# Kernel tuning notes

Hardware: AMD Instinct MI355X
Metric: run time of the kernel (lower is better)

Reference implementation:

```python
import jax, jax.numpy as jnp
import numpy as np

# Spec constants (from init_kwargs)
NUM_ANCHORS = 5
NUM_CLASSES = 80
FM_H = 19
FM_W = 19
MAX_OBJECT = 50
NOOBJECT_SCALE = 1.0
OBJECT_SCALE = 5.0
BACKGROUND_THRESHOLD = 0.6
COORD_SCALE = 1.0
CLASS_SCALE = 1.0


def _iou_cwh(a, b):
    """IoU for boxes in (cx, cy, w, h) format; broadcasts over leading dims.
    Matches bbox_iou(..., x1y1x2y2=False) in the torch repo (0 when no overlap)."""
    ax1, ax2 = a[..., 0] - a[..., 2] * 0.5, a[..., 0] + a[..., 2] * 0.5
    ay1, ay2 = a[..., 1] - a[..., 3] * 0.5, a[..., 1] + a[..., 3] * 0.5
    bx1, bx2 = b[..., 0] - b[..., 2] * 0.5, b[..., 0] + b[..., 2] * 0.5
    by1, by2 = b[..., 1] - b[..., 3] * 0.5, b[..., 1] + b[..., 3] * 0.5
    uw = jnp.maximum(ax2, bx2) - jnp.minimum(ax1, bx1)
    uh = jnp.maximum(ay2, by2) - jnp.minimum(ay1, by1)
    cw = a[..., 2] + b[..., 2] - uw
    ch = a[..., 3] + b[..., 3] - uh
    inter = jnp.where((cw > 0) & (ch > 0), cw * ch, 0.0)
    union = a[..., 2] * a[..., 3] + b[..., 2] * b[..., 3] - inter
    return inter / jnp.maximum(union, 1e-12)


def setup_inputs() -> dict:
    key = jax.random.key(0)
    k1, k2, k3, k4, k5 = jax.random.split(key, 5)
    B, A, C, H, W, T = 64, NUM_ANCHORS, NUM_CLASSES, FM_H, FM_W, MAX_OBJECT
    output = jax.random.normal(k1, (B, A * (5 + C), H, W), jnp.float32) * 0.5
    # targets: per object (class, cx, cy, w, h), normalized to [0,1]; list ends at first cx == 0
    cls_t = jax.random.randint(k2, (B, T), 0, C).astype(jnp.float32)
    xy = jax.random.uniform(k3, (B, T, 2), jnp.float32, minval=0.1, maxval=0.9)
    wh = jax.random.uniform(k4, (B, T, 2), jnp.float32, minval=0.05, maxval=0.4)
    nvalid = jax.random.randint(k5, (B,), 1, T + 1)
    valid = (jnp.arange(T)[None, :] < nvalid[:, None]).astype(jnp.float32)
    tgt = jnp.concatenate([cls_t[..., None], xy, wh], axis=-1) * valid[..., None]
    target = tgt.reshape(B, T * 5)
    anchors = jnp.array([[1.3221, 1.73145], [3.19275, 4.00944], [5.05587, 8.09892],
                         [9.47112, 4.84053], [11.2364, 10.0071]], jnp.float32)
    return {"output": output, "target": target, "anchors": anchors}


def reference(output, target, anchors):
    B = output.shape[0]
    A, C, H, W, T = NUM_ANCHORS, NUM_CLASSES, FM_H, FM_W, MAX_OBJECT
    out = output.reshape(B, A, 5 + C, H, W)
    x = jax.nn.sigmoid(out[:, :, 0])
    y = jax.nn.sigmoid(out[:, :, 1])
    w = out[:, :, 2]
    h = out[:, :, 3]
    conf = jax.nn.sigmoid(out[:, :, 4])
    cls_logits = jnp.transpose(out[:, :, 5:], (0, 1, 3, 4, 2))  # [B,A,H,W,C]

    # decoded predicted boxes in grid units (detached for target building, as in torch)
    px = x + jnp.arange(W, dtype=x.dtype)[None, None, None, :]
    py = y + jnp.arange(H, dtype=x.dtype)[None, None, :, None]
    pw = jnp.exp(w) * anchors[None, :, 0, None, None]
    ph = jnp.exp(h) * anchors[None, :, 1, None, None]
    pred = jax.lax.stop_gradient(jnp.stack([px, py, pw, ph], axis=-1))  # [B,A,H,W,4]

    tgt = target.reshape(B, T, 5)
    cls_t = tgt[..., 0]
    gx = tgt[..., 1] * W
    gy = tgt[..., 2] * H
    gw = tgt[..., 3] * W
    gh = tgt[..., 4] * H
    # break-at-first-zero semantics of the torch loop
    valid = jnp.cumprod((tgt[..., 1] != 0).astype(jnp.int32), axis=1).astype(bool)  # [B,T]

    gt_boxes = jnp.stack([gx, gy, gw, gh], axis=-1)  # [B,T,4]
    # all-pairs pred-vs-gt IoU (replaces per-object python loop)
    pred_flat = pred.reshape(B, A * H * W, 4)
    ious = _iou_cwh(pred_flat[:, :, None, :], gt_boxes[:, None, :, :])  # [B,N,T]
    best_iou = jnp.max(jnp.where(valid[:, None, :], ious, 0.0), axis=-1)  # [B,N]
    conf_mask = jnp.where(best_iou > BACKGROUND_THRESHOLD, 0.0, NOOBJECT_SCALE)
    conf_mask = conf_mask.reshape(B, A, H, W)

    # best anchor per gt: IoU of (w,h) boxes centered at origin
    aw = anchors[:, 0][None, None, :]
    ah = anchors[:, 1][None, None, :]
    inter_a = jnp.minimum(gw[..., None], aw) * jnp.minimum(gh[..., None], ah)
    union_a = gw[..., None] * gh[..., None] + aw * ah - inter_a
    best_n = jnp.argmax(inter_a / jnp.maximum(union_a, 1e-12), axis=-1)  # [B,T]

    gi = jnp.clip(gx.astype(jnp.int32), 0, W - 1)
    gj = jnp.clip(gy.astype(jnp.int32), 0, H - 1)
    bidx = jnp.arange(B)[:, None]
    pred_sel = pred[bidx, best_n, gj, gi]  # [B,T,4]
    iou_obj = _iou_cwh(gt_boxes, pred_sel)  # [B,T]

    N = B * A * H * W
    flat = ((bidx * A + best_n) * H + gj) * W + gi  # [B,T]
    flat = jnp.where(valid, flat, N).reshape(-1)  # invalid -> out of range, dropped

    def scat(vals):
        return jnp.zeros((N,), jnp.float32).at[flat].set(
            vals.reshape(-1), mode="drop").reshape(B, A, H, W)

    coord_mask = scat(jnp.ones_like(gx))
    cls_mask = coord_mask
    conf_mask = conf_mask.reshape(-1).at[flat].set(
        jnp.full((B * T,), OBJECT_SCALE, jnp.float32), mode="drop").reshape(B, A, H, W)
    tx = scat(gx - gi.astype(gx.dtype))
    ty = scat(gy - gj.astype(gy.dtype))
    tw = scat(jnp.log(jnp.maximum(gw, 1e-12) / anchors[best_n, 0]))
    th = scat(jnp.log(jnp.maximum(gh, 1e-12) / anchors[best_n, 1]))
    tconf = scat(iou_obj)
    tcls = scat(cls_t)

    # losses (sum reduction, matching MSELoss/CrossEntropyLoss(size_average=False))
    loss_x = COORD_SCALE * jnp.sum((coord_mask * (x - tx)) ** 2) / 2.0
    loss_y = COORD_SCALE * jnp.sum((coord_mask * (y - ty)) ** 2) / 2.0
    loss_w = COORD_SCALE * jnp.sum((coord_mask * (w - tw)) ** 2) / 2.0
    loss_h = COORD_SCALE * jnp.sum((coord_mask * (h - th)) ** 2) / 2.0
    sq = jnp.sqrt(conf_mask)
    loss_conf = jnp.sum((sq * (conf - tconf)) ** 2) / 2.0
    ce = -jnp.take_along_axis(jax.nn.log_softmax(cls_logits, axis=-1),
                              tcls.astype(jnp.int32)[..., None], axis=-1)[..., 0]
    loss_cls = CLASS_SCALE * jnp.sum(cls_mask * ce)
    return loss_x + loss_y + loss_w + loss_h + loss_conf + loss_cls
```

## Files before the change

### kernel.cpp

```cpp
#include <hip/hip_runtime.h>
#include <math.h>

#define NUM_ANCHORS 5
#define NUM_CLASSES 80
#define FM_H 19
#define FM_W 19
#define MAX_OBJECT 50
#define HW (FM_H * FM_W)
#define CELLS_PER_B (NUM_ANCHORS * HW)
#define CH (5 + NUM_CLASSES)
#define BLOCKS_PER_B ((CELLS_PER_B + 255) / 256)
#define NOOBJECT_SCALE 1.0f
#define OBJECT_SCALE 5.0f
#define BACKGROUND_THRESHOLD 0.6f

struct GTEntry {
    float gx, gy, gw, gh;
    float tx, ty, tw, th;
    int   acell;
    int   cls;
};

__device__ inline float frcp(float v) { return __builtin_amdgcn_rcpf(v); }
__device__ inline float fsigmoid(float v) { return frcp(1.0f + __expf(-v)); }

__device__ inline float iou_cwh(float ax, float ay, float aw, float ah,
                                float bx, float by, float bw, float bh) {
    float ax1 = ax - aw * 0.5f, ax2 = ax + aw * 0.5f;
    float ay1 = ay - ah * 0.5f, ay2 = ay + ah * 0.5f;
    float bx1 = bx - bw * 0.5f, bx2 = bx + bw * 0.5f;
    float by1 = by - bh * 0.5f, by2 = by + bh * 0.5f;
    float uw = fmaxf(ax2, bx2) - fminf(ax1, bx1);
    float uh = fmaxf(ay2, by2) - fminf(ay1, by1);
    float cw = aw + bw - uw;
    float chh = ah + bh - uh;
    float inter = (cw > 0.0f && chh > 0.0f) ? cw * chh : 0.0f;
    float uni = aw * ah + bw * bh - inter;
    return inter * frcp(fmaxf(uni, 1e-12f));
}

__global__ __launch_bounds__(256) void yolov2_main(
    const float* __restrict__ out,
    const float* __restrict__ target,
    const float* __restrict__ anchors,
    float* __restrict__ partial)
{
    const int b    = blockIdx.x / BLOCKS_PER_B;
    const int blk  = blockIdx.x % BLOCKS_PER_B;
    const int cell = blk * 256 + threadIdx.x;
    const int lane = threadIdx.x & 63;
    const int wid  = threadIdx.x >> 6;

    __shared__ float tg[MAX_OBJECT * 5];
    __shared__ float anc[NUM_ANCHORS * 2];
    __shared__ GTEntry g[MAX_OBJECT];
    __shared__ int   nv_sh;
    __shared__ int   n_obj;
    __shared__ int   entries[MAX_OBJECT];
    __shared__ float wsum[4];

    for (int i = threadIdx.x; i < MAX_OBJECT * 5; i += blockDim.x)
        tg[i] = target[b * MAX_OBJECT * 5 + i];
    if (threadIdx.x < NUM_ANCHORS * 2)
        anc[threadIdx.x] = anchors[threadIdx.x];
    if (threadIdx.x == 0) n_obj = 0;
    __syncthreads();

    if (threadIdx.x < 64) {
        unsigned long long m =
            __ballot(threadIdx.x < MAX_OBJECT && tg[threadIdx.x * 5 + 1] != 0.0f);
        if (threadIdx.x == 0) nv_sh = __popcll(m);
    }

    if (threadIdx.x < MAX_OBJECT) {
        const int t = threadIdx.x;
        float cls = tg[t * 5 + 0];
        float gx = tg[t * 5 + 1] * (float)FM_W;
        float gy = tg[t * 5 + 2] * (float)FM_H;
        float gw = tg[t * 5 + 3] * (float)FM_W;
        float gh = tg[t * 5 + 4] * (float)FM_H;
        int bn = 0; float best = -1.0f;
        #pragma unroll
        for (int a = 0; a < NUM_ANCHORS; ++a) {
            float aw = anc[2 * a], ah = anc[2 * a + 1];
            float inter = fminf(gw, aw) * fminf(gh, ah);
            float uni = gw * gh + aw * ah - inter;
            float r = inter * frcp(fmaxf(uni, 1e-12f));
            if (r > best) { best = r; bn = a; }
        }
        int gi = (int)gx; gi = gi < 0 ? 0 : (gi > FM_W - 1 ? FM_W - 1 : gi);
        int gj = (int)gy; gj = gj < 0 ? 0 : (gj > FM_H - 1 ? FM_H - 1 : gj);
        GTEntry e;
        e.gx = gx; e.gy = gy; e.gw = gw; e.gh = gh;
        e.tx = gx - (float)gi;
        e.ty = gy - (float)gj;
        e.tw = logf(fmaxf(gw, 1e-12f) * frcp(anc[2 * bn]));
        e.th = logf(fmaxf(gh, 1e-12f) * frcp(anc[2 * bn + 1]));
        e.acell = bn * HW + gj * FM_W + gi;
        e.cls = (int)cls;
        g[t] = e;
    }
    __syncthreads();

    const int nv = nv_sh;

    float local = 0.0f;
    if (cell < CELLS_PER_B) {
        const int a  = cell / HW;
        const int hw = cell - a * HW;
        const int hrow = hw / FM_W;
        const int wcol = hw - hrow * FM_W;

        const float* base = out + ((size_t)b * NUM_ANCHORS * CH + (size_t)a * CH) * HW + hw;
        float ox = base[0 * HW];
        float oy = base[1 * HW];
        float ow = base[2 * HW];
        float oh = base[3 * HW];
        float oc = base[4 * HW];

        float x = fsigmoid(ox);
        float y = fsigmoid(oy);
        float conf = fsigmoid(oc);
        float px = x + (float)wcol;
        float py = y + (float)hrow;
        float pw = __expf(ow) * anc[2 * a];
        float ph = __expf(oh) * anc[2 * a + 1];

        float best_iou = 0.0f;
        int   last_t = -1;
        float tconf = 0.0f;
        #pragma unroll 5
        for (int t = 0; t < nv; ++t) {
            float iou = iou_cwh(g[t].gx, g[t].gy, g[t].gw, g[t].gh, px, py, pw, ph);
            best_iou = fmaxf(best_iou, iou);
            bool match = (g[t].acell == cell);
            last_t = match ? t : last_t;
            tconf  = match ? iou : tconf;
        }

        if (last_t >= 0) {
            float dc = conf - tconf;
            local += 0.5f * OBJECT_SCALE * dc * dc;
            float dx = x  - g[last_t].tx; local += 0.5f * dx * dx;
            float dy = y  - g[last_t].ty; local += 0.5f * dy * dy;
            float dw = ow - g[last_t].tw; local += 0.5f * dw * dw;
            float dh = oh - g[last_t].th; local += 0.5f * dh * dh;
            int pos = atomicAdd(&n_obj, 1);
            entries[pos] = cell | (g[last_t].cls << 16);
        } else {
            if (!(best_iou > BACKGROUND_THRESHOLD))
                local += 0.5f * NOOBJECT_SCALE * conf * conf;
        }
    }
    __syncthreads();

    const int ne = n_obj;
    for (int e = wid; e < ne; e += 4) {
        int pk    = entries[e];
        int ecell = pk & 0xFFFF;
        int ecls  = pk >> 16;
        int a  = ecell / HW;
        int hw = ecell - a * HW;
        const float* cl = out + ((size_t)b * NUM_ANCHORS * CH + (size_t)a * CH + 5) * HW + hw;
        float v0 = (lane < NUM_CLASSES / 2) ? cl[(2 * lane + 0) * HW] : -INFINITY;
        float v1 = (lane < NUM_CLASSES / 2) ? cl[(2 * lane + 1) * HW] : -INFINITY;
        float tl = cl[(size_t)ecls * HW];
        float m = fmaxf(v0, v1);
        #pragma unroll
        for (int off = 32; off > 0; off >>= 1)
            m = fmaxf(m, __shfl_xor(m, off, 64));
        float s = (lane < NUM_CLASSES / 2)
                    ? (__expf(v0 - m) + __expf(v1 - m)) : 0.0f;
        #pragma unroll
        for (int off = 32; off > 0; off >>= 1)
            s += __shfl_xor(s, off, 64);
        if (lane == 0) local += (m + __logf(s) - tl);
    }

    for (int off = 32; off > 0; off >>= 1)
        local += __shfl_down(local, off, 64);
    if (lane == 0) wsum[wid] = local;
    __syncthreads();
    if (threadIdx.x == 0)
        partial[blockIdx.x] = wsum[0] + wsum[1] + wsum[2] + wsum[3];
}

__global__ __launch_bounds__(256) void yolov2_reduce(
    const float* __restrict__ partial, int n, float* __restrict__ loss)
{
    __shared__ float wsum[4];
    float v = 0.0f;
    for (int i = threadIdx.x; i < n; i += 256) v += partial[i];
    for (int off = 32; off > 0; off >>= 1)
        v += __shfl_down(v, off, 64);
    const int lane = threadIdx.x & 63;
    const int wid  = threadIdx.x >> 6;
    if (lane == 0) wsum[wid] = v;
    __syncthreads();
    if (threadIdx.x == 0) loss[0] = wsum[0] + wsum[1] + wsum[2] + wsum[3];
}

extern "C" void kernel_launch(void* const* d_in, const int* in_sizes, int n_in,
                              void* d_out, int out_size, void* d_ws, size_t ws_size,
                              hipStream_t stream) {
    const float* out_t   = (const float*)d_in[0];
    const float* target  = (const float*)d_in[1];
    const float* anchors = (const float*)d_in[2];
    float* loss    = (float*)d_out;
    float* partial = (float*)d_ws;

    const int B = in_sizes[1] / (MAX_OBJECT * 5);
    const int nblocks = B * BLOCKS_PER_B;

    yolov2_main<<<dim3(nblocks), dim3(256), 0, stream>>>(out_t, target, anchors, partial);
    yolov2_reduce<<<dim3(1), dim3(256), 0, stream>>>(partial, nblocks, loss);
}
```

Baseline: 18.79 us.

## Hoist cell loads before GT setup and precompute box corners in LDS

Each thread now issues its five prediction loads and anchor reads before the ground-truth preprocessing, so global latency overlaps with target setup. That setup also reads target directly into registers, which removes one barrier and the staging buffer. Ground-truth boxes are stored as packed float4 corners, sizes and areas, and the IoU loop becomes a division-free threshold compare, with the full IoU computed only for the matched cell. The target class logit is taken by a shuffle instead of an extra global load. Changing `iou > 0.6` to `inter > 0.6*uni` may differ slightly in rounding at the threshold boundary.

```diff
diff --git a/kernel.cpp b/kernel.cpp
--- a/kernel.cpp
+++ b/kernel.cpp
@@ -10,34 +10,11 @@
 #define CELLS_PER_B (NUM_ANCHORS * HW)
 #define CH (5 + NUM_CLASSES)
 #define BLOCKS_PER_B ((CELLS_PER_B + 255) / 256)
-#define NOOBJECT_SCALE 1.0f
 #define OBJECT_SCALE 5.0f
 #define BACKGROUND_THRESHOLD 0.6f
 
-struct GTEntry {
-    float gx, gy, gw, gh;
-    float tx, ty, tw, th;
-    int   acell;
-    int   cls;
-};
-
 __device__ inline float frcp(float v) { return __builtin_amdgcn_rcpf(v); }
 __device__ inline float fsigmoid(float v) { return frcp(1.0f + __expf(-v)); }
-
-__device__ inline float iou_cwh(float ax, float ay, float aw, float ah,
-                                float bx, float by, float bw, float bh) {
-    float ax1 = ax - aw * 0.5f, ax2 = ax + aw * 0.5f;
-    float ay1 = ay - ah * 0.5f, ay2 = ay + ah * 0.5f;
-    float bx1 = bx - bw * 0.5f, bx2 = bx + bw * 0.5f;
-    float by1 = by - bh * 0.5f, by2 = by + bh * 0.5f;
-    float uw = fmaxf(ax2, bx2) - fminf(ax1, bx1);
-    float uh = fmaxf(ay2, by2) - fminf(ay1, by1);
-    float cw = aw + bw - uw;
-    float chh = ah + bh - uh;
-    float inter = (cw > 0.0f && chh > 0.0f) ? cw * chh : 0.0f;
-    float uni = aw * ah + bw * bh - inter;
-    return inter * frcp(fmaxf(uni, 1e-12f));
-}
 
 __global__ __launch_bounds__(256) void yolov2_main(
     const float* __restrict__ out,
@@ -51,105 +28,121 @@
     const int lane = threadIdx.x & 63;
     const int wid  = threadIdx.x >> 6;
 
-    __shared__ float tg[MAX_OBJECT * 5];
-    __shared__ float anc[NUM_ANCHORS * 2];
-    __shared__ GTEntry g[MAX_OBJECT];
-    __shared__ int   nv_sh;
-    __shared__ int   n_obj;
-    __shared__ int   entries[MAX_OBJECT];
-    __shared__ float wsum[4];
-
-    for (int i = threadIdx.x; i < MAX_OBJECT * 5; i += blockDim.x)
-        tg[i] = target[b * MAX_OBJECT * 5 + i];
-    if (threadIdx.x < NUM_ANCHORS * 2)
-        anc[threadIdx.x] = anchors[threadIdx.x];
+    __shared__ float4 gA[MAX_OBJECT];
+    __shared__ float4 gB[MAX_OBJECT];
+    __shared__ float4 gT[MAX_OBJECT];
+    __shared__ int    gcls[MAX_OBJECT];
+    __shared__ int    nv_sh, n_obj;
+    __shared__ int    entries[MAX_OBJECT];
+    __shared__ float  wsum[4];
+
+    const bool incell = (cell < CELLS_PER_B);
+    const int a    = incell ? (cell / HW) : 0;
+    const int hw   = cell - a * HW;
+    const int hrow = hw / FM_W;
+    const int wcol = hw - hrow * FM_W;
+
+    const float* base = out + ((size_t)(b * NUM_ANCHORS + a) * CH) * HW + hw;
+    float ox = 0.f, oy = 0.f, ow = 0.f, oh = 0.f, oc = 0.f;
+    if (incell) {
+        ox = base[0];
+        oy = base[HW];
+        ow = base[2 * HW];
+        oh = base[3 * HW];
+        oc = base[4 * HW];
+    }
+    const float anc_w = anchors[2 * a];
+    const float anc_h = anchors[2 * a + 1];
+
     if (threadIdx.x == 0) n_obj = 0;
-    __syncthreads();
 
     if (threadIdx.x < 64) {
-        unsigned long long m =
-            __ballot(threadIdx.x < MAX_OBJECT && tg[threadIdx.x * 5 + 1] != 0.0f);
-        if (threadIdx.x == 0) nv_sh = __popcll(m);
-    }
-
-    if (threadIdx.x < MAX_OBJECT) {
         const int t = threadIdx.x;
-        float cls = tg[t * 5 + 0];
-        float gx = tg[t * 5 + 1] * (float)FM_W;
-        float gy = tg[t * 5 + 2] * (float)FM_H;
-        float gw = tg[t * 5 + 3] * (float)FM_W;
-        float gh = tg[t * 5 + 4] * (float)FM_H;
-        int bn = 0; float best = -1.0f;
-        #pragma unroll
-        for (int a = 0; a < NUM_ANCHORS; ++a) {
-            float aw = anc[2 * a], ah = anc[2 * a + 1];
-            float inter = fminf(gw, aw) * fminf(gh, ah);
-            float uni = gw * gh + aw * ah - inter;
-            float r = inter * frcp(fmaxf(uni, 1e-12f));
-            if (r > best) { best = r; bn = a; }
-        }
-        int gi = (int)gx; gi = gi < 0 ? 0 : (gi > FM_W - 1 ? FM_W - 1 : gi);
-        int gj = (int)gy; gj = gj < 0 ? 0 : (gj > FM_H - 1 ? FM_H - 1 : gj);
-        GTEntry e;
-        e.gx = gx; e.gy = gy; e.gw = gw; e.gh = gh;
-        e.tx = gx - (float)gi;
-        e.ty = gy - (float)gj;
-        e.tw = logf(fmaxf(gw, 1e-12f) * frcp(anc[2 * bn]));
-        e.th = logf(fmaxf(gh, 1e-12f) * frcp(anc[2 * bn + 1]));
-        e.acell = bn * HW + gj * FM_W + gi;
-        e.cls = (int)cls;
-        g[t] = e;
+        float f0 = 0.f, f1 = 0.f, f2 = 0.f, f3 = 0.f, f4 = 0.f;
+        if (t < MAX_OBJECT) {
+            const float* tp = target + (size_t)b * MAX_OBJECT * 5 + t * 5;
+            f0 = tp[0]; f1 = tp[1]; f2 = tp[2]; f3 = tp[3]; f4 = tp[4];
+        }
+        unsigned long long m = __ballot(t < MAX_OBJECT && f1 != 0.0f);
+        if (t == 0) nv_sh = __popcll(m);
+        if (t < MAX_OBJECT) {
+            float gx = f1 * (float)FM_W;
+            float gy = f2 * (float)FM_H;
+            float gw = f3 * (float)FM_W;
+            float gh = f4 * (float)FM_H;
+            int bn = 0; float best = -1.0f;
+            #pragma unroll
+            for (int k = 0; k < NUM_ANCHORS; ++k) {
+                float aw = anchors[2 * k], ah = anchors[2 * k + 1];
+                float inter = fminf(gw, aw) * fminf(gh, ah);
+                float uni = gw * gh + aw * ah - inter;
+                float r = inter * frcp(fmaxf(uni, 1e-12f));
+                if (r > best) { best = r; bn = k; }
+            }
+            int gi = (int)gx; gi = gi < 0 ? 0 : (gi > FM_W - 1 ? FM_W - 1 : gi);
+            int gj = (int)gy; gj = gj < 0 ? 0 : (gj > FM_H - 1 ? FM_H - 1 : gj);
+            int acell = bn * HW + gj * FM_W + gi;
+            gA[t] = make_float4(gx - gw * 0.5f, gx + gw * 0.5f,
+                                gy - gh * 0.5f, gy + gh * 0.5f);
+            gB[t] = make_float4(gw, gh, gw * gh, __int_as_float(acell));
+            gT[t] = make_float4(gx - (float)gi, gy - (float)gj,
+                                logf(fmaxf(gw, 1e-12f) * frcp(anchors[2 * bn])),
+                                logf(fmaxf(gh, 1e-12f) * frcp(anchors[2 * bn + 1])));
+            gcls[t] = (int)f0;
+        }
     }
     __syncthreads();
 
     const int nv = nv_sh;
-
     float local = 0.0f;
-    if (cell < CELLS_PER_B) {
-        const int a  = cell / HW;
-        const int hw = cell - a * HW;
-        const int hrow = hw / FM_W;
-        const int wcol = hw - hrow * FM_W;
-
-        const float* base = out + ((size_t)b * NUM_ANCHORS * CH + (size_t)a * CH) * HW + hw;
-        float ox = base[0 * HW];
-        float oy = base[1 * HW];
-        float ow = base[2 * HW];
-        float oh = base[3 * HW];
-        float oc = base[4 * HW];
-
-        float x = fsigmoid(ox);
-        float y = fsigmoid(oy);
+
+    if (incell) {
+        float x    = fsigmoid(ox);
+        float y    = fsigmoid(oy);
         float conf = fsigmoid(oc);
         float px = x + (float)wcol;
         float py = y + (float)hrow;
-        float pw = __expf(ow) * anc[2 * a];
-        float ph = __expf(oh) * anc[2 * a + 1];
-
-        float best_iou = 0.0f;
-        int   last_t = -1;
-        float tconf = 0.0f;
+        float pw = __expf(ow) * anc_w;
+        float ph = __expf(oh) * anc_h;
+        float ax1 = px - pw * 0.5f, ax2 = px + pw * 0.5f;
+        float ay1 = py - ph * 0.5f, ay2 = py + ph * 0.5f;
+        float parea = pw * ph;
+
+        bool bg_hit = false;
+        int  last_t = -1;
         #pragma unroll 5
         for (int t = 0; t < nv; ++t) {
-            float iou = iou_cwh(g[t].gx, g[t].gy, g[t].gw, g[t].gh, px, py, pw, ph);
-            best_iou = fmaxf(best_iou, iou);
-            bool match = (g[t].acell == cell);
-            last_t = match ? t : last_t;
-            tconf  = match ? iou : tconf;
+            float4 A  = gA[t];
+            float4 Bv = gB[t];
+            float uw = fmaxf(ax2, A.y) - fminf(ax1, A.x);
+            float uh = fmaxf(ay2, A.w) - fminf(ay1, A.z);
+            float cw  = Bv.x + pw - uw;
+            float chh = Bv.y + ph - uh;
+            float inter = (cw > 0.f && chh > 0.f) ? cw * chh : 0.f;
+            float uni = parea + Bv.z - inter;
+            bg_hit = bg_hit || (inter > BACKGROUND_THRESHOLD * uni);
+            if (__float_as_int(Bv.w) == cell) last_t = t;
         }
 
         if (last_t >= 0) {
-            float dc = conf - tconf;
-            local += 0.5f * OBJECT_SCALE * dc * dc;
-            float dx = x  - g[last_t].tx; local += 0.5f * dx * dx;
-            float dy = y  - g[last_t].ty; local += 0.5f * dy * dy;
-            float dw = ow - g[last_t].tw; local += 0.5f * dw * dw;
-            float dh = oh - g[last_t].th; local += 0.5f * dh * dh;
+            float4 A  = gA[last_t];
+            float4 Bv = gB[last_t];
+            float4 Tt = gT[last_t];
+            float uw = fmaxf(ax2, A.y) - fminf(ax1, A.x);
+            float uh = fmaxf(ay2, A.w) - fminf(ay1, A.z);
+            float cw  = Bv.x + pw - uw;
+            float chh = Bv.y + ph - uh;
+            float inter = (cw > 0.f && chh > 0.f) ? cw * chh : 0.f;
+            float tconf = inter * frcp(fmaxf(parea + Bv.z - inter, 1e-12f));
+            float dc = conf - tconf; local += 0.5f * OBJECT_SCALE * dc * dc;
+            float dx = x  - Tt.x; local += 0.5f * dx * dx;
+            float dy = y  - Tt.y; local += 0.5f * dy * dy;
+            float dw = ow - Tt.z; local += 0.5f * dw * dw;
+            float dh = oh - Tt.w; local += 0.5f * dh * dh;
             int pos = atomicAdd(&n_obj, 1);
-            entries[pos] = cell | (g[last_t].cls << 16);
-        } else {
-            if (!(best_iou > BACKGROUND_THRESHOLD))
-                local += 0.5f * NOOBJECT_SCALE * conf * conf;
+            entries[pos] = cell | (gcls[last_t] << 16);
+        } else if (!bg_hit) {
+            local += 0.5f * conf * conf;
         }
     }
     __syncthreads();
@@ -159,12 +152,11 @@
         int pk    = entries[e];
         int ecell = pk & 0xFFFF;
         int ecls  = pk >> 16;
-        int a  = ecell / HW;
-        int hw = ecell - a * HW;
-        const float* cl = out + ((size_t)b * NUM_ANCHORS * CH + (size_t)a * CH + 5) * HW + hw;
+        int ea  = ecell / HW;
+        int ehw = ecell - ea * HW;
+        const float* cl = out + ((size_t)(b * NUM_ANCHORS + ea) * CH + 5) * HW + ehw;
         float v0 = (lane < NUM_CLASSES / 2) ? cl[(2 * lane + 0) * HW] : -INFINITY;
         float v1 = (lane < NUM_CLASSES / 2) ? cl[(2 * lane + 1) * HW] : -INFINITY;
-        float tl = cl[(size_t)ecls * HW];
         float m = fmaxf(v0, v1);
         #pragma unroll
         for (int off = 32; off > 0; off >>= 1)
@@ -174,9 +166,12 @@
         #pragma unroll
         for (int off = 32; off > 0; off >>= 1)
             s += __shfl_xor(s, off, 64);
+        float tsel = (ecls & 1) ? v1 : v0;
+        float tl = __shfl(tsel, ecls >> 1, 64);
         if (lane == 0) local += (m + __logf(s) - tl);
     }
 
+    #pragma unroll
     for (int off = 32; off > 0; off >>= 1)
         local += __shfl_down(local, off, 64);
     if (lane == 0) wsum[wid] = local;
@@ -191,6 +186,7 @@
     __shared__ float wsum[4];
     float v = 0.0f;
     for (int i = threadIdx.x; i < n; i += 256) v += partial[i];
+    #pragma unroll
     for (int off = 32; off > 0; off >>= 1)
         v += __shfl_down(v, off, 64);
     const int lane = threadIdx.x & 63;
```

New measurement: 18.76 us. Within noise of the previous version (-0.1%).
